# Kernel optimization log

Measured on AMD Instinct MI355X. Metric: run time of the kernel, lower is better.

The kernel has to match this reference:

```python
import jax, jax.numpy as jnp
import numpy as np

D_MODEL = 768
N_HEADS = 12
D_HEAD = 64
INIT_RANGE = 0.02
IGNORE = -100000.0


def setup_inputs() -> dict:
    key = jax.random.key(0)
    ks = jax.random.split(key, 5)
    x = jax.random.normal(ks[0], (2, 2048, D_MODEL), dtype=jnp.float32)
    W_Q = INIT_RANGE * jax.random.normal(ks[1], (N_HEADS, D_MODEL, D_HEAD), dtype=jnp.float32)
    W_K = INIT_RANGE * jax.random.normal(ks[2], (N_HEADS, D_MODEL, D_HEAD), dtype=jnp.float32)
    W_V = INIT_RANGE * jax.random.normal(ks[3], (N_HEADS, D_MODEL, D_HEAD), dtype=jnp.float32)
    W_O = INIT_RANGE * jax.random.normal(ks[4], (N_HEADS, D_HEAD, D_MODEL), dtype=jnp.float32)
    b_Q = jnp.zeros((N_HEADS, D_HEAD), dtype=jnp.float32)
    b_K = jnp.zeros((N_HEADS, D_HEAD), dtype=jnp.float32)
    b_V = jnp.zeros((N_HEADS, D_HEAD), dtype=jnp.float32)
    b_O = jnp.zeros((D_MODEL,), dtype=jnp.float32)
    return {"x": x, "W_Q": W_Q, "b_Q": b_Q, "W_K": W_K, "b_K": b_K,
            "W_V": W_V, "b_V": b_V, "W_O": W_O, "b_O": b_O}


def reference(x, W_Q, b_Q, W_K, b_K, W_V, b_V, W_O, b_O):
    # x: [b, s, m]; W_*: [h, m, d]
    Q = jnp.einsum('bsm,hmd->bshd', x, W_Q) + b_Q  # [b, s, h, d]
    K = jnp.einsum('bsm,hmd->bshd', x, W_K) + b_K
    V = jnp.einsum('bsm,hmd->bshd', x, W_V) + b_V
    scores = jnp.einsum('bqhd,bkhd->bhqk', Q, K) / jnp.sqrt(jnp.float32(D_HEAD))
    s = scores.shape[-1]
    causal = jnp.triu(jnp.ones((s, s), dtype=bool), k=1)  # True above diagonal
    scores = jnp.where(causal, jnp.float32(IGNORE), scores)
    pattern = jax.nn.softmax(scores, axis=-1)  # [b, h, q, k]
    Z = jnp.einsum('bhqk,bkhd->bqhd', pattern, V)
    out = jnp.einsum('bqhd,hdm->bqm', Z, W_O) + b_O
    return out
```

## Files before the change

### kernel.cpp

```cpp
#include <hip/hip_runtime.h>
#include <hip/hip_bf16.h>

#define BATCH 2
#define SLEN 2048
#define NH 12
#define DM 768
#define DH 64
#define ROWS (BATCH*SLEN)
#define NQKV (3*DM)
#define NCHUNK 40

typedef __attribute__((ext_vector_type(8))) short bf16x8;
typedef __attribute__((ext_vector_type(4))) float f32x4;
typedef __attribute__((ext_vector_type(16))) float f32x16;
typedef unsigned short u16;
typedef unsigned int u32;
typedef __attribute__((ext_vector_type(4))) unsigned short u16x4;
typedef __attribute__((ext_vector_type(8))) unsigned short u16x8;

__device__ __forceinline__ u16 f2b(float f) {
    unsigned int u = __builtin_bit_cast(unsigned int, f);
    unsigned int r = (u + 0x7FFFu + ((u >> 16) & 1u)) >> 16;
    return (u16)r;
}
__device__ __forceinline__ float b2f(u16 v) {
    unsigned int u = ((unsigned int)v) << 16;
    return __builtin_bit_cast(float, u);
}

__device__ __forceinline__ void gload16(const u16* g, u16* l) {
    __builtin_amdgcn_global_load_lds(
        (const __attribute__((address_space(1))) unsigned int*)g,
        (__attribute__((address_space(3))) unsigned int*)l,
        16, 0, 0);
}


__global__ __launch_bounds__(256) void pack_all(const float* __restrict__ x,
                                                const float* __restrict__ WQ, const float* __restrict__ WK,
                                                const float* __restrict__ WV, const float* __restrict__ WO,
                                                u16* __restrict__ xb, u16* __restrict__ wqkv,
                                                u16* __restrict__ wo) {
    __shared__ u16 L[64 * 72];
    int blk = blockIdx.x;
    int t = threadIdx.x;
    if (blk < 1536) {
        int i = blk * 256 + t;
        const float4* xv = (const float4*)x;
        float4 a = xv[i * 2], b = xv[i * 2 + 1];
        u16x8 o;
        o[0] = f2b(a.x); o[1] = f2b(a.y); o[2] = f2b(a.z); o[3] = f2b(a.w);
        o[4] = f2b(b.x); o[5] = f2b(b.y); o[6] = f2b(b.z); o[7] = f2b(b.w);
        *(u16x8*)(xb + (size_t)i * 8) = o;
    } else if (blk < 1968) {
        int idx = blk - 1536;
        int mt = idx % 12, h = (idx / 12) % 12, sel = idx / 144;
        const float* W = sel == 0 ? WQ : (sel == 1 ? WK : WV);
        const float* src = W + ((size_t)h * DM + mt * 64) * DH;
        for (int j = 0; j < 4; j++) {
            int i = t + 256 * j;
            int r = i >> 4, cf = i & 15;
            float4 v = ((const float4*)src)[i];
            u16x4 o; o[0] = f2b(v.x); o[1] = f2b(v.y); o[2] = f2b(v.z); o[3] = f2b(v.w);
            *(u16x4*)&L[r * 72 + cf * 4] = o;
        }
        __syncthreads();
        u16* orow = wqkv + ((size_t)(sel * DM + h * DH)) * DM + mt * 64;
        for (int j = 0; j < 16; j++) {
            int e = t + 256 * j;
            int d = e >> 6, mm = e & 63;
            orow[(size_t)d * DM + mm] = L[mm * 72 + d];
        }
    } else {
        int idx = blk - 1968;
        int bi = idx % 12, bj = idx / 12;
        for (int j = 0; j < 4; j++) {
            int i = t + 256 * j;
            int r = i >> 4, cf = i & 15;
            float4 v = ((const float4*)(WO + (size_t)(bi * 64 + r) * DM + bj * 64))[cf];
            u16x4 o; o[0] = f2b(v.x); o[1] = f2b(v.y); o[2] = f2b(v.z); o[3] = f2b(v.w);
            *(u16x4*)&L[r * 72 + cf * 4] = o;
        }
        __syncthreads();
        for (int j = 0; j < 16; j++) {
            int e = t + 256 * j;
            int c = e >> 6, r = e & 63;
            wo[(size_t)(bj * 64 + c) * DM + bi * 64 + r] = L[r * 72 + c];
        }
    }
}


__global__ __launch_bounds__(256) void gemm_qkv(const u16* __restrict__ A, const u16* __restrict__ Bt,
                                                const float* __restrict__ bQ, const float* __restrict__ bK,
                                                const float* __restrict__ bV,
                                                u16* __restrict__ Qb, u16* __restrict__ Kb, u16* __restrict__ Vb) {
    __shared__ u16 S[128 * 64 + 96 * 64];
    u16* Al = S;
    u16* Bl = S + 128 * 64;
    int t = threadIdx.x;
    int n0 = blockIdx.x * 96, m0 = blockIdx.y * 128;
    int lane = t & 63, w = t >> 6;
    int ln = lane & 15, qd = lane >> 4;
    int wr = (w & 1) * 64, wc = (w >> 1) * 48;
    int srow = lane >> 3, slot = lane & 7;
    f32x4 acc[4][3] = {};

    for (int kt = 0; kt < DM / 64; kt++) {
        __syncthreads();
        for (int j = 0; j < 4; j++) {
            int r = w * 32 + j * 8 + srow;
            int gc = slot ^ (r & 7);
            gload16(A + (size_t)(m0 + r) * DM + kt * 64 + gc * 8, &Al[(w * 32 + j * 8) * 64]);
        }
        for (int j = 0; j < 3; j++) {
            int r = w * 24 + j * 8 + srow;
            int gc = slot ^ (r & 7);
            gload16(Bt + (size_t)(n0 + r) * DM + kt * 64 + gc * 8, &Bl[(w * 24 + j * 8) * 64]);
        }
        __syncthreads();
        for (int ks = 0; ks < 2; ks++) {
            int sl = ((ks * 4 + qd) ^ (ln & 7)) * 8;
            bf16x8 af[4], bfr[3];
            for (int rt = 0; rt < 4; rt++)
                af[rt] = *(const bf16x8*)&Al[(wr + rt * 16 + ln) * 64 + sl];
            for (int ct = 0; ct < 3; ct++)
                bfr[ct] = *(const bf16x8*)&Bl[(wc + ct * 16 + ln) * 64 + sl];
            for (int rt = 0; rt < 4; rt++)
                for (int ct = 0; ct < 3; ct++)
                    acc[rt][ct] = __builtin_amdgcn_mfma_f32_16x16x32_bf16(af[rt], bfr[ct], acc[rt][ct], 0, 0, 0);
        }
    }
    int sel = n0 / DM;
    if (sel == 2) {
        __syncthreads();
        for (int ct = 0; ct < 3; ct++) {
            int c = wc + ct * 16 + ln;
            float bv = bV[n0 - 2 * DM + c];
            for (int rt = 0; rt < 4; rt++) {
                int s = wr + rt * 16 + qd * 4;
                for (int r = 0; r < 4; r++)
                    S[c * 136 + s + r] = f2b(acc[rt][ct][r] + bv);
            }
        }
        __syncthreads();
        int bb = m0 >> 11, ss0 = m0 & 2047;
        for (int it = 0; it < 6; it++) {
            int e = t + it * 256;
            int c = e >> 4, ck = e & 15;
            int gcol = n0 - 2 * DM + c;
            int hh = gcol >> 6, dd = gcol & 63;
            u16x8 v = *(const u16x8*)&S[c * 136 + ck * 8];
            *(u16x8*)&Vb[(((size_t)bb * NH + hh) * DH + dd) * SLEN + ss0 + ck * 8] = v;
        }
    } else {
        const float* bias = sel == 0 ? bQ : bK;
        u16* Out = sel == 0 ? Qb : Kb;
        const float qs = sel == 0 ? 0.125f * 1.44269504f : 1.0f;
        for (int ct = 0; ct < 3; ct++) {
            int col = n0 - sel * DM + wc + ct * 16 + ln;
            int hh = col >> 6, dd = col & 63;
            float bv = bias[col];
            for (int rt = 0; rt < 4; rt++) {
                int row = m0 + wr + rt * 16 + qd * 4;
                for (int r = 0; r < 4; r++) {
                    int rg = row + r;
                    int bb = rg >> 11, ss = rg & 2047;
                    Out[(((size_t)bb * NH + hh) * SLEN + ss) * DH + dd] = f2b((acc[rt][ct][r] + bv) * qs);
                }
            }
        }
    }
}


__device__ __forceinline__ void cid2qc(int cid, int& qt, int& c, int& nc) {
    if (cid < 4)       { qt = cid;                   c = 0;               nc = 1; }
    else if (cid < 12) { qt = 4 + ((cid - 4) >> 1);  c = (cid - 4) & 1;   nc = 2; }
    else if (cid < 24) { qt = 8 + (cid - 12) / 3;    c = (cid - 12) % 3;  nc = 3; }
    else               { qt = 12 + ((cid - 24) >> 2); c = (cid - 24) & 3; nc = 4; }
}

__global__ __launch_bounds__(256, 3) void attn(const u16* __restrict__ Qb, const u16* __restrict__ Kb,
                                               const u16* __restrict__ Vtg,
                                               u16* __restrict__ Po, float* __restrict__ Plv) {
    __shared__ u16 Kl[2][64 * 64];
    __shared__ u16 Vt[2][64 * 64];
    __shared__ u16 Pq[4][32 * 64];
    int blk = blockIdx.x;
    int cid = (NCHUNK - 1) - blk / 24;
    int j24 = blk % 24;
    int bh = (j24 & 7) * 3 + (j24 >> 3);
    int qt, c, nc;
    cid2qc(cid, qt, c, nc);
    int ntiles = 2 * qt + 2;
    int kt0 = c * ntiles / nc, kt1 = (c + 1) * ntiles / nc;
    const u16* Qp = Qb + (size_t)bh * SLEN * DH;
    const u16* Kp = Kb + (size_t)bh * SLEN * DH;
    const u16* Vp = Vtg + (size_t)bh * SLEN * DH;
    int t = threadIdx.x, lane = t & 63, w = t >> 6;
    int l31 = lane & 31, h = lane >> 5;
    int qg = qt * 128 + w * 32 + l31;
    int srow = lane >> 3, slot = lane & 7;
    int sw = (l31 & 7) << 3;

    bf16x8 qf[4];
    for (int ks = 0; ks < 4; ks++)
        qf[ks] = *(const bf16x8*)(Qp + (size_t)qg * DH + ks * 16 + h * 8);

    f32x16 o[2] = {};
    float lsum = 0.f;
    u16* Pw = Pq[w];

    auto stage = [&](int kt, int buf) {
        int k0 = kt * 64;
        for (int j = 0; j < 2; j++) {
            int r = w * 16 + j * 8 + srow;
            int gc = slot ^ (r & 7);
            gload16(Kp + (size_t)(k0 + r) * DH + gc * 8, &Kl[buf][(w * 16 + j * 8) * 64]);
            gload16(Vp + (size_t)r * SLEN + k0 + gc * 8, &Vt[buf][(w * 16 + j * 8) * 64]);
        }
    };

    stage(kt0, 0);
    __syncthreads();
    int cur = 0;
    for (int kt = kt0; kt < kt1; kt++) {
        int k0 = kt * 64;
        if (kt + 1 < kt1) stage(kt + 1, cur ^ 1);
        const u16* Kc = Kl[cur];
        const u16* Vc = Vt[cur];

        for (int kb = 0; kb < 2; kb++) {
            f32x16 sf = {};
            for (int ks = 0; ks < 4; ks++) {
                int row = kb * 32 + l31;
                bf16x8 kf = *(const bf16x8*)&Kc[row * 64 + (((ks * 2 + h) ^ (row & 7)) * 8)];
                sf = __builtin_amdgcn_mfma_f32_32x32x16_bf16(kf, qf[ks], sf, 0, 0, 0);
            }
            if (k0 + 63 > qt * 128 + w * 32) {
                for (int r = 0; r < 16; r++) {
                    int kg = k0 + kb * 32 + (r & 3) + 8 * (r >> 2) + 4 * h;
                    if (kg > qg) sf[r] = -1e30f;
                }
            }
            u32 pr[8];
            for (int p = 0; p < 8; p++) {
                u32 e0 = __builtin_bit_cast(u32, exp2f(sf[2 * p]));
                u32 e1 = __builtin_bit_cast(u32, exp2f(sf[2 * p + 1]));
                pr[p] = __builtin_amdgcn_perm(e1, e0, 0x07060302u);
            }
            for (int p = 0; p < 8; p++) {
                lsum += __builtin_bit_cast(float, pr[p] << 16);
                lsum += __builtin_bit_cast(float, pr[p] & 0xFFFF0000u);
            }
            {
                uint2 s;
                s.x = pr[0]; s.y = pr[1];
                *(uint2*)&Pw[l31 * 64 + ((kb * 32 + 4 * h) ^ sw)] = s;
                s.x = pr[2]; s.y = pr[3];
                *(uint2*)&Pw[l31 * 64 + ((kb * 32 + 8 + 4 * h) ^ sw)] = s;
                s.x = pr[4]; s.y = pr[5];
                *(uint2*)&Pw[l31 * 64 + ((kb * 32 + 16 + 4 * h) ^ sw)] = s;
                s.x = pr[6]; s.y = pr[7];
                *(uint2*)&Pw[l31 * 64 + ((kb * 32 + 24 + 4 * h) ^ sw)] = s;
            }
            for (int cc = 0; cc < 2; cc++) {
                bf16x8 pf = *(const bf16x8*)&Pw[l31 * 64 + ((kb * 32 + cc * 16 + 8 * h) ^ sw)];
                int ch4 = kb * 2 + cc;
                for (int db = 0; db < 2; db++) {
                    int row = db * 32 + l31;
                    bf16x8 vf = *(const bf16x8*)&Vc[row * 64 + (((ch4 * 2 + h) ^ (row & 7)) * 8)];
                    o[db] = __builtin_amdgcn_mfma_f32_32x32x16_bf16(vf, pf, o[db], 0, 0, 0);
                }
            }
        }
        __syncthreads();
        cur ^= 1;
    }

    size_t pid = (size_t)bh * NCHUNK + cid;
    u16* op = Po + pid * (128 * 64);
    for (int db = 0; db < 2; db++)
        for (int rq = 0; rq < 4; rq++) {
            u16x4 ov;
            for (int j = 0; j < 4; j++) ov[j] = f2b(o[db][rq * 4 + j]);
            *(u16x4*)&op[(w * 32 + l31) * 64 + db * 32 + rq * 8 + 4 * h] = ov;
        }
    lsum += __shfl_xor(lsum, 32, 64);
    if (h == 0)
        Plv[pid * 128 + w * 32 + l31] = lsum;
}


__global__ __launch_bounds__(256) void combine(const u16* __restrict__ Po, const float* __restrict__ Plv,
                                               u16* __restrict__ Zb) {
    int qtile = blockIdx.x, bh = blockIdx.y;
    int b = bh / NH, hH = bh % NH;
    int nc = qtile < 4 ? 1 : (qtile < 8 ? 2 : (qtile < 12 ? 3 : 4));
    int base = qtile < 4 ? qtile
             : (qtile < 8 ? 4 + (qtile - 4) * 2
             : (qtile < 12 ? 12 + (qtile - 8) * 3
                           : 24 + (qtile - 12) * 4));
    int t = threadIdx.x;
    int q = t >> 1, dseg = (t & 1) * 32;

    float acc[32] = {};
    float lsum = 0.f;
    for (int cc = 0; cc < nc; cc++) {
        size_t pid = (size_t)bh * NCHUNK + base + cc;
        lsum += Plv[pid * 128 + q];
        const u16* op = Po + pid * (128 * 64) + q * 64 + dseg;
        for (int jj = 0; jj < 4; jj++) {
            u16x8 v = *(const u16x8*)(op + jj * 8);
            for (int e = 0; e < 8; e++)
                acc[jj * 8 + e] += b2f(v[e]);
        }
    }
    float inv = 1.0f / lsum;
    u16* Zp = Zb + ((size_t)b * SLEN + qtile * 128 + q) * DM + hH * DH + dseg;
    for (int jj = 0; jj < 4; jj++) {
        u16x8 ov;
        for (int e = 0; e < 8; e++) ov[e] = f2b(acc[jj * 8 + e] * inv);
        *(u16x8*)(Zp + jj * 8) = ov;
    }
}


__global__ __launch_bounds__(256) void gemm_proj(const u16* __restrict__ A, const u16* __restrict__ Bt,
                                                 const float* __restrict__ bO, float* __restrict__ out) {
    __shared__ u16 Al[64 * 64];
    __shared__ u16 Bl[96 * 64];
    int t = threadIdx.x;
    int n0 = blockIdx.x * 96, m0 = blockIdx.y * 64;
    int lane = t & 63, w = t >> 6;
    int ln = lane & 15, qd = lane >> 4;
    int wr = (w & 1) * 32, wc = (w >> 1) * 48;
    int srow = lane >> 3, slot = lane & 7;
    f32x4 acc[2][3] = {};

    for (int kt = 0; kt < DM / 64; kt++) {
        __syncthreads();
        for (int j = 0; j < 2; j++) {
            int r = w * 16 + j * 8 + srow;
            int gc = slot ^ (r & 7);
            gload16(A + (size_t)(m0 + r) * DM + kt * 64 + gc * 8, &Al[(w * 16 + j * 8) * 64]);
        }
        for (int j = 0; j < 3; j++) {
            int r = w * 24 + j * 8 + srow;
            int gc = slot ^ (r & 7);
            gload16(Bt + (size_t)(n0 + r) * DM + kt * 64 + gc * 8, &Bl[(w * 24 + j * 8) * 64]);
        }
        __syncthreads();
        for (int ks = 0; ks < 2; ks++) {
            int sl = ((ks * 4 + qd) ^ (ln & 7)) * 8;
            bf16x8 af[2], bfr[3];
            for (int rt = 0; rt < 2; rt++)
                af[rt] = *(const bf16x8*)&Al[(wr + rt * 16 + ln) * 64 + sl];
            for (int ct = 0; ct < 3; ct++)
                bfr[ct] = *(const bf16x8*)&Bl[(wc + ct * 16 + ln) * 64 + sl];
            for (int rt = 0; rt < 2; rt++)
                for (int ct = 0; ct < 3; ct++)
                    acc[rt][ct] = __builtin_amdgcn_mfma_f32_16x16x32_bf16(af[rt], bfr[ct], acc[rt][ct], 0, 0, 0);
        }
    }
    for (int ct = 0; ct < 3; ct++) {
        int col = n0 + wc + ct * 16 + ln;
        float bv = bO[col];
        for (int rt = 0; rt < 2; rt++) {
            int row = m0 + wr + rt * 16 + qd * 4;
            for (int r = 0; r < 4; r++)
                out[(size_t)(row + r) * DM + col] = acc[rt][ct][r] + bv;
        }
    }
}


extern "C" void kernel_launch(void* const* d_in, const int* in_sizes, int n_in,
                              void* d_out, int out_size, void* d_ws, size_t ws_size,
                              hipStream_t stream) {
    const float* x  = (const float*)d_in[0];
    const float* WQ = (const float*)d_in[1];
    const float* bQ = (const float*)d_in[2];
    const float* WK = (const float*)d_in[3];
    const float* bK = (const float*)d_in[4];
    const float* WV = (const float*)d_in[5];
    const float* bV = (const float*)d_in[6];
    const float* WO = (const float*)d_in[7];
    const float* bO = (const float*)d_in[8];
    float* out = (float*)d_out;

    u16* xb   = (u16*)d_ws;
    u16* wqkv = xb + (size_t)ROWS * DM;
    u16* wo   = wqkv + (size_t)NQKV * DM;
    u16* Qb   = wo + (size_t)DM * DM;
    size_t hsz = (size_t)BATCH * NH * SLEN * DH;
    u16* Kb   = Qb + hsz;
    u16* Vb   = Kb + hsz;
    u16* Zb   = Vb + hsz;
    u16* Po   = Zb + (size_t)ROWS * DM;
    float* Pl = (float*)(Po + (size_t)BATCH * NH * NCHUNK * 128 * 64);

    pack_all<<<2112, 256, 0, stream>>>(x, WQ, WK, WV, WO, xb, wqkv, wo);
    gemm_qkv<<<dim3(NQKV / 96, ROWS / 128), 256, 0, stream>>>(xb, wqkv, bQ, bK, bV, Qb, Kb, Vb);
    attn<<<dim3(NCHUNK * 24), 256, 0, stream>>>(Qb, Kb, Vb, Po, Pl);
    combine<<<dim3(SLEN / 128, BATCH * NH), 256, 0, stream>>>(Po, Pl, Zb);
    gemm_proj<<<dim3(DM / 96, ROWS / 64), 256, 0, stream>>>(Zb, wo, bO, out);
}
```

Baseline: 165.2 us.

## Fuse split-KV combine into output projection GEMM and shrink attention P scratch

Removes the separate combine kernel: gemm_proj now reads the partial attention outputs and row sums directly, sums the chunks, normalizes by the reciprocal sum and writes the A tile into shared memory, so the Z intermediate is never written to global memory. The attention kernel's per-warp P buffer is halved, with a matching swizzle, to allow four blocks per CU. The projection grid is remapped to a 1D launch grouped by XCD. The cost is redundant chunk summation across the 8 column blocks and synchronous global loads in the GEMM A path.

```diff
diff --git a/kernel.cpp b/kernel.cpp
--- a/kernel.cpp
+++ b/kernel.cpp
@@ -181,12 +181,12 @@
     else               { qt = 12 + ((cid - 24) >> 2); c = (cid - 24) & 3; nc = 4; }
 }
 
-__global__ __launch_bounds__(256, 3) void attn(const u16* __restrict__ Qb, const u16* __restrict__ Kb,
+__global__ __launch_bounds__(256, 4) void attn(const u16* __restrict__ Qb, const u16* __restrict__ Kb,
                                                const u16* __restrict__ Vtg,
                                                u16* __restrict__ Po, float* __restrict__ Plv) {
     __shared__ u16 Kl[2][64 * 64];
     __shared__ u16 Vt[2][64 * 64];
-    __shared__ u16 Pq[4][32 * 64];
+    __shared__ u16 Pq[4][32 * 32];
     int blk = blockIdx.x;
     int cid = (NCHUNK - 1) - blk / 24;
     int j24 = blk % 24;
@@ -202,7 +202,7 @@
     int l31 = lane & 31, h = lane >> 5;
     int qg = qt * 128 + w * 32 + l31;
     int srow = lane >> 3, slot = lane & 7;
-    int sw = (l31 & 7) << 3;
+    int sw = (l31 & 3) << 3;
 
     bf16x8 qf[4];
     for (int ks = 0; ks < 4; ks++)
@@ -257,16 +257,16 @@
             {
                 uint2 s;
                 s.x = pr[0]; s.y = pr[1];
-                *(uint2*)&Pw[l31 * 64 + ((kb * 32 + 4 * h) ^ sw)] = s;
+                *(uint2*)&Pw[l31 * 32 + ((4 * h) ^ sw)] = s;
                 s.x = pr[2]; s.y = pr[3];
-                *(uint2*)&Pw[l31 * 64 + ((kb * 32 + 8 + 4 * h) ^ sw)] = s;
+                *(uint2*)&Pw[l31 * 32 + ((8 + 4 * h) ^ sw)] = s;
                 s.x = pr[4]; s.y = pr[5];
-                *(uint2*)&Pw[l31 * 64 + ((kb * 32 + 16 + 4 * h) ^ sw)] = s;
+                *(uint2*)&Pw[l31 * 32 + ((16 + 4 * h) ^ sw)] = s;
                 s.x = pr[6]; s.y = pr[7];
-                *(uint2*)&Pw[l31 * 64 + ((kb * 32 + 24 + 4 * h) ^ sw)] = s;
+                *(uint2*)&Pw[l31 * 32 + ((24 + 4 * h) ^ sw)] = s;
             }
             for (int cc = 0; cc < 2; cc++) {
-                bf16x8 pf = *(const bf16x8*)&Pw[l31 * 64 + ((kb * 32 + cc * 16 + 8 * h) ^ sw)];
+                bf16x8 pf = *(const bf16x8*)&Pw[l31 * 32 + ((cc * 16 + 8 * h) ^ sw)];
                 int ch4 = kb * 2 + cc;
                 for (int db = 0; db < 2; db++) {
                     int row = db * 32 + l31;
@@ -293,58 +293,53 @@
 }
 
 
-__global__ __launch_bounds__(256) void combine(const u16* __restrict__ Po, const float* __restrict__ Plv,
-                                               u16* __restrict__ Zb) {
-    int qtile = blockIdx.x, bh = blockIdx.y;
-    int b = bh / NH, hH = bh % NH;
+__global__ __launch_bounds__(256) void gemm_proj(const u16* __restrict__ Po, const float* __restrict__ Plv,
+                                                 const u16* __restrict__ Bt, const float* __restrict__ bO,
+                                                 float* __restrict__ out) {
+    __shared__ u16 Al[64 * 64];
+    __shared__ u16 Bl[96 * 64];
+    __shared__ float Linv[12][64];
+    int blk = blockIdx.x;
+    int xcd = blk & 7, idx = blk >> 3;
+    int by = xcd * 8 + (idx >> 3), bx = idx & 7;
+    int n0 = bx * 96, m0 = by * 64;
+    int b = m0 >> 11, qtile = (m0 >> 7) & 15, qh = m0 & 127;
     int nc = qtile < 4 ? 1 : (qtile < 8 ? 2 : (qtile < 12 ? 3 : 4));
     int base = qtile < 4 ? qtile
              : (qtile < 8 ? 4 + (qtile - 4) * 2
              : (qtile < 12 ? 12 + (qtile - 8) * 3
                            : 24 + (qtile - 12) * 4));
     int t = threadIdx.x;
-    int q = t >> 1, dseg = (t & 1) * 32;
-
-    float acc[32] = {};
-    float lsum = 0.f;
-    for (int cc = 0; cc < nc; cc++) {
-        size_t pid = (size_t)bh * NCHUNK + base + cc;
-        lsum += Plv[pid * 128 + q];
-        const u16* op = Po + pid * (128 * 64) + q * 64 + dseg;
-        for (int jj = 0; jj < 4; jj++) {
-            u16x8 v = *(const u16x8*)(op + jj * 8);
-            for (int e = 0; e < 8; e++)
-                acc[jj * 8 + e] += b2f(v[e]);
-        }
-    }
-    float inv = 1.0f / lsum;
-    u16* Zp = Zb + ((size_t)b * SLEN + qtile * 128 + q) * DM + hH * DH + dseg;
-    for (int jj = 0; jj < 4; jj++) {
-        u16x8 ov;
-        for (int e = 0; e < 8; e++) ov[e] = f2b(acc[jj * 8 + e] * inv);
-        *(u16x8*)(Zp + jj * 8) = ov;
-    }
-}
-
-
-__global__ __launch_bounds__(256) void gemm_proj(const u16* __restrict__ A, const u16* __restrict__ Bt,
-                                                 const float* __restrict__ bO, float* __restrict__ out) {
-    __shared__ u16 Al[64 * 64];
-    __shared__ u16 Bl[96 * 64];
-    int t = threadIdx.x;
-    int n0 = blockIdx.x * 96, m0 = blockIdx.y * 64;
     int lane = t & 63, w = t >> 6;
     int ln = lane & 15, qd = lane >> 4;
     int wr = (w & 1) * 32, wc = (w >> 1) * 48;
     int srow = lane >> 3, slot = lane & 7;
     f32x4 acc[2][3] = {};
 
+    for (int j = 0; j < 3; j++) {
+        int e = t + 256 * j;
+        int hh = e >> 6, q = e & 63;
+        size_t pidb = ((size_t)(b * NH + hh)) * NCHUNK + base;
+        float ls = 0.f;
+        for (int cc = 0; cc < nc; cc++) ls += Plv[(pidb + cc) * 128 + qh + q];
+        Linv[hh][q] = 1.0f / ls;
+    }
+
     for (int kt = 0; kt < DM / 64; kt++) {
         __syncthreads();
+        size_t pidb = ((size_t)(b * NH + kt)) * NCHUNK + base;
         for (int j = 0; j < 2; j++) {
-            int r = w * 16 + j * 8 + srow;
-            int gc = slot ^ (r & 7);
-            gload16(A + (size_t)(m0 + r) * DM + kt * 64 + gc * 8, &Al[(w * 16 + j * 8) * 64]);
+            int r = (t >> 3) + 32 * j;
+            int c8 = (t & 7) * 8;
+            float a[8] = {};
+            for (int cc = 0; cc < nc; cc++) {
+                u16x8 v = *(const u16x8*)(Po + (pidb + cc) * (128 * 64) + (size_t)(qh + r) * 64 + c8);
+                for (int e = 0; e < 8; e++) a[e] += b2f(v[e]);
+            }
+            float il = Linv[kt][r];
+            u16x8 ov;
+            for (int e = 0; e < 8; e++) ov[e] = f2b(a[e] * il);
+            *(u16x8*)&Al[r * 64 + (((t & 7) ^ (r & 7)) * 8)] = ov;
         }
         for (int j = 0; j < 3; j++) {
             int r = w * 24 + j * 8 + srow;
@@ -397,13 +392,11 @@
     size_t hsz = (size_t)BATCH * NH * SLEN * DH;
     u16* Kb   = Qb + hsz;
     u16* Vb   = Kb + hsz;
-    u16* Zb   = Vb + hsz;
-    u16* Po   = Zb + (size_t)ROWS * DM;
+    u16* Po   = Vb + hsz;
     float* Pl = (float*)(Po + (size_t)BATCH * NH * NCHUNK * 128 * 64);
 
     pack_all<<<2112, 256, 0, stream>>>(x, WQ, WK, WV, WO, xb, wqkv, wo);
     gemm_qkv<<<dim3(NQKV / 96, ROWS / 128), 256, 0, stream>>>(xb, wqkv, bQ, bK, bV, Qb, Kb, Vb);
     attn<<<dim3(NCHUNK * 24), 256, 0, stream>>>(Qb, Kb, Vb, Po, Pl);
-    combine<<<dim3(SLEN / 128, BATCH * NH), 256, 0, stream>>>(Po, Pl, Zb);
-    gemm_proj<<<dim3(DM / 96, ROWS / 64), 256, 0, stream>>>(Zb, wo, bO, out);
-}
+    gemm_proj<<<512, 256, 0, stream>>>(Po, Pl, wo, bO, out);
+}
```

New measurement: 182.3 us. 10.4% more time.
